# Kernel tuning notes

Hardware: AMD Instinct MI355X
Metric: run time of the kernel (lower is better)

The kernel has to match this reference:

```python
import jax, jax.numpy as jnp
import numpy as np

N, D, DEG, DEPTH, H = 50000, 300, 6, 3, 4
E = N * DEG
DK = D // H


def setup_inputs() -> dict:
    key = jax.random.key(0)
    ks = jax.random.split(key, 14)
    # circulant molecular-like graph: node i <-> i+k (k=1,2,3), edges emitted in
    # reverse pairs (2t, 2t+1) as required by reverse_edge()
    u = np.arange(N)
    src_l, dst_l = [], []
    for k in (1, 2, 3):
        v = (u + k) % N
        src_l.append(np.stack([u, v], 1).reshape(-1))
        dst_l.append(np.stack([v, u], 1).reshape(-1))
    src = np.concatenate(src_l).astype(np.int32)
    dst = np.concatenate(dst_l).astype(np.int32)
    # incoming-edge ids per node (every node has exactly DEG in-edges)
    order = np.argsort(dst, kind='stable')
    nbr_eids = order.reshape(N, DEG).astype(np.int32)
    nbr_mask = np.ones((N, DEG), dtype=bool)
    sd = 1.0 / np.sqrt(D)
    p = lambda i, shape: jax.random.normal(ks[i], shape, jnp.float32) * sd
    return {
        'f': jax.random.normal(ks[0], (N, D), jnp.float32),
        'x': jax.random.normal(ks[1], (E, D), jnp.float32),
        'Wq': p(2, (D, D)), 'bq': jnp.zeros((D,), jnp.float32),
        'Wk': p(3, (D, D)), 'bk': jnp.zeros((D,), jnp.float32),
        'Wv': p(4, (D, D)), 'bv': jnp.zeros((D,), jnp.float32),
        'Wo': p(5, (D, D)), 'bo': jnp.zeros((D,), jnp.float32),
        'W_mp': p(6, (DEPTH - 1, D, D)), 'b_mp': jnp.zeros((DEPTH - 1, D), jnp.float32),
        'W_last': p(7, (3 * D, D)), 'b_last': jnp.zeros((D,), jnp.float32),
        'src': jnp.asarray(src), 'dst': jnp.asarray(dst),
        'nbr_eids': jnp.asarray(nbr_eids), 'nbr_mask': jnp.asarray(nbr_mask),
    }


def reference(f, x, Wq, bq, Wk, bk, Wv, bv, Wo, bo, W_mp, b_mp, W_last, b_last,
              src, dst, nbr_eids, nbr_mask):
    n = f.shape[0]
    e = x.shape[0]
    rev = jnp.arange(e) ^ 1                     # reverse-pair permutation
    has_in = nbr_mask.any(axis=-1)              # [N]
    scale = 1.0 / jnp.sqrt(jnp.float32(DK))
    h = x                                       # edge state 'h' init from 'x'
    f_h = f                                     # node state 'f_h' init from 'f'
    for i in range(DEPTH - 1):
        # ragged mailbox of incoming edge states, padded to DEG
        m = jnp.where(nbr_mask[..., None], h[nbr_eids], 0.0)        # [N,DEG,D]
        q = (f_h @ Wq + bq).reshape(n, H, DK)                        # query = node feat
        k = (m @ Wk + bk).reshape(n, DEG, H, DK)                     # key   = mailbox
        v = ((m + f_h[:, None, :]) @ Wv + bv).reshape(n, DEG, H, DK) # value = mailbox + feat
        scores = jnp.einsum('nhk,ndhk->nhd', q, k) * scale          # [N,H,DEG]
        scores = jnp.where(nbr_mask[:, None, :], scores, -1e9)
        attn = jax.nn.softmax(scores, axis=-1)
        out = jnp.einsum('nhd,ndhk->nhk', attn, v).reshape(n, D) @ Wo + bo
        f_h = jnp.where(has_in[:, None], out, f_h)
        # edge update: m = f_h[src] - rev_h; h = relu(x + Linear_i(m))
        m_e = f_h[src] - h[rev]
        h = jax.nn.relu(x + m_e @ W_mp[i] + b_mp[i])
    # GEANet is undefined in the provided source -> identity pass-through
    mail = jax.ops.segment_sum(h, dst, num_segments=n)              # sum of in-edge states
    f_new = jnp.concatenate([mail, f_h, f], axis=-1) @ W_last + b_last
    f_final = jnp.where(has_in[:, None], f_new, f_h)
    return f_final, h
```

## Files before the change

kernel.cpp:

```cpp
#include <hip/hip_runtime.h>
#include <hip/hip_bf16.h>

typedef unsigned long long ull;
typedef unsigned int u32;
typedef unsigned short u16;
typedef __hip_bfloat16 bf16;
typedef __attribute__((ext_vector_type(8))) short v8s;
typedef __attribute__((ext_vector_type(4))) float v4f;
typedef __attribute__((ext_vector_type(2))) ull v2u;

#define NN 50000
#define DD 300
#define PD 320
#define EE (NN*6)

__device__ __forceinline__ u16 f2bf(float f) {
    u32 u = __float_as_uint(f);
    u32 r = u + 0x7FFFu + ((u >> 16) & 1u);
    return (u16)(r >> 16);
}
__device__ __forceinline__ u32 cvtpk(float lo, float hi) {
    u32 r;
    asm("v_cvt_pk_bf16_f32 %0, %1, %2" : "=v"(r) : "v"(lo), "v"(hi));
    return r;
}
__device__ __forceinline__ float lo16(u32 u) { return __uint_as_float(u << 16); }
__device__ __forceinline__ float hi16(u32 u) { return __uint_as_float(u & 0xffff0000u); }

__device__ __forceinline__ u32 sub2bf(u32 a, u32 b) {
    return cvtpk(lo16(a) - lo16(b), hi16(a) - hi16(b));
}
__device__ __forceinline__ ull sub4bf(ull a, ull b) {
    u32 l = sub2bf((u32)a, (u32)b);
    u32 h = sub2bf((u32)(a >> 32), (u32)(b >> 32));
    return (ull)l | ((ull)h << 32);
}

enum { A_DIR = 0, A_MPG = 1, A_CAT = 2 };
enum { E_BIAS = 0, E_RELUX = 1 };
enum { O_F32 = 1, O_BF16 = 2, O_BOTH = 3 };

template<int AMODE, int EPI, int OUTM, int NW, int NSEG>
__global__ __launch_bounds__(NW*64)
void gemm_mfma(const bf16* __restrict__ A0, const bf16* __restrict__ A1,
               const bf16* __restrict__ A2, const bf16* __restrict__ A3,
               const bf16* __restrict__ A4,
               const int* __restrict__ srcidx, const bf16* __restrict__ BT,
               const float* __restrict__ bias0, const float* __restrict__ bias1,
               const bf16* __restrict__ xepi,
               float* __restrict__ Cf, bf16* __restrict__ Cb0, bf16* __restrict__ Cb1,
               int M, int ybias, long ycb)
{
    __shared__ __align__(16) char Als[64 * 640];
    const int tid = threadIdx.x;
    const int wave = tid >> 6, lane = tid & 63;
    const int l15 = lane & 15, l4 = lane >> 4;
    const int wv = (NW == 8) ? (wave & 3) : wave;
    const int half = (NW == 8) ? (wave >> 2) : 0;
    const int rowBase = blockIdx.x * 64;
    const int T = NW * 64;
    const int gy = blockIdx.y;
    BT += (long)gy * 204800;
    if (bias0) bias0 += (long)gy * ybias;
    if (bias1) bias1 += (long)gy * ybias;
    if (Cb0) Cb0 += gy * ycb;
    if (Cb1) Cb1 += gy * ycb;

    v4f acc[4][5];
    const v4f vzero = {0.f, 0.f, 0.f, 0.f};
    #pragma unroll
    for (int mt = 0; mt < 4; ++mt)
        #pragma unroll
        for (int nt = 0; nt < 5; ++nt) acc[mt][nt] = vzero;

    for (int seg = 0; seg < NSEG; ++seg) {
        const bf16* As = (seg == 0) ? A0 : (seg == 1 ? A1 : (seg == 2 ? A2 :
                         (seg == 3 ? A3 : A4)));
        if (seg) __syncthreads();
        #pragma unroll
        for (int s = 0; s < 2560 / T; ++s) {
            int c = tid + T * s;
            int r = c / 40, ch = c - r * 40;
            int grow = rowBase + r;
            int gc = (grow < M) ? grow : 0;
            v2u v;
            if (AMODE == A_MPG) {
                int s0 = srcidx[gc];
                v2u a = *(const v2u*)(A0 + (long)s0 * PD + ch * 8);
                v2u b = *(const v2u*)(A1 + (long)(gc ^ 1) * PD + ch * 8);
                v[0] = sub4bf(a[0], b[0]);
                v[1] = sub4bf(a[1], b[1]);
            } else {
                v = *(const v2u*)(As + (long)gc * PD + ch * 8);
            }
            *(v2u*)(Als + ((c * 16) ^ ((r & 7) << 4))) = v;
        }
        __syncthreads();

        const bf16* BTs = BT + (long)seg * 320 * PD;
        #pragma unroll
        for (int ks = 0; ks < 10; ++ks) {
            v8s af[4];
            #pragma unroll
            for (int mt = 0; mt < 4; ++mt) {
                int rowL = mt * 16 + l15;
                af[mt] = *(const v8s*)(Als +
                    ((rowL * 640 + ks * 64 + l4 * 16) ^ ((rowL & 7) << 4)));
            }
            #pragma unroll
            for (int nt = 0; nt < 5; ++nt) {
                int col = wave * 80 + nt * 16 + l15;
                v8s bfr = *(const v8s*)(BTs + (long)col * PD + ks * 32 + l4 * 8);
                #pragma unroll
                for (int mt = 0; mt < 4; ++mt)
                    acc[mt][nt] = __builtin_amdgcn_mfma_f32_16x16x32_bf16(
                        af[mt], bfr, acc[mt][nt], 0, 0, 0);
            }
        }
        if (seg + 1 < NSEG) __syncthreads();
    }

    const int NOUT = (NW == 8) ? 2 : 1;
    #pragma unroll
    for (int oh = 0; oh < NOUT; ++oh) {
        __syncthreads();
        if (half == oh) {
            const float* bias = oh ? bias1 : bias0;
            #pragma unroll
            for (int nt = 0; nt < 5; ++nt) {
                int col = wv * 80 + nt * 16 + l15;
                float bvv = bias ? bias[col] : 0.f;
                #pragma unroll
                for (int mt = 0; mt < 4; ++mt) {
                    #pragma unroll
                    for (int r = 0; r < 4; ++r) {
                        int rowL = mt * 16 + l4 * 4 + r;
                        *(u16*)(Als + ((rowL * 640 + col * 2) ^ (((rowL >> 2) & 7) << 4)))
                            = f2bf(acc[mt][nt][r] + bvv);
                    }
                }
            }
        }
        __syncthreads();
        {
            bf16* Cb = oh ? Cb1 : Cb0;
            #pragma unroll
            for (int s = 0; s < 2560 / T; ++s) {
                int c = tid + T * s;
                int r = c / 40, ch = c - r * 40;
                int grow = rowBase + r;
                if (grow >= M) continue;
                v2u val = *(const v2u*)(Als + ((c * 16) ^ (((r >> 2) & 7) << 4)));
                if (EPI == E_RELUX) {
                    v2u xv = *(const v2u*)(xepi + (long)grow * PD + ch * 8);
                    #pragma unroll
                    for (int w = 0; w < 2; ++w) {
                        u32 a0 = (u32)val[w], a1 = (u32)(val[w] >> 32);
                        u32 x0 = (u32)xv[w],  x1 = (u32)(xv[w] >> 32);
                        u32 r0 = cvtpk(fmaxf(lo16(a0) + lo16(x0), 0.f),
                                       fmaxf(hi16(a0) + hi16(x0), 0.f));
                        u32 r1 = cvtpk(fmaxf(lo16(a1) + lo16(x1), 0.f),
                                       fmaxf(hi16(a1) + hi16(x1), 0.f));
                        val[w] = (ull)r0 | ((ull)r1 << 32);
                    }
                }
                if (OUTM & O_BF16)
                    *(v2u*)(Cb + (long)grow * PD + ch * 8) = val;
                if (OUTM & O_F32) {
                    int col0 = ch * 8;
                    if (col0 < DD) {
                        u32 a0 = (u32)val[0], a1 = (u32)(val[0] >> 32);
                        float4 lo = {lo16(a0), hi16(a0), lo16(a1), hi16(a1)};
                        *(float4*)(Cf + (long)grow * DD + col0) = lo;
                        if (col0 + 4 < DD) {
                            u32 b0 = (u32)val[1], b1 = (u32)(val[1] >> 32);
                            float4 hi = {lo16(b0), hi16(b0), lo16(b1), hi16(b1)};
                            *(float4*)(Cf + (long)grow * DD + col0 + 4) = hi;
                        }
                    }
                }
            }
        }
    }
}

__global__ __launch_bounds__(256)
void scoreU_k(const bf16* __restrict__ G0, const bf16* __restrict__ G1,
              const bf16* __restrict__ G2, const bf16* __restrict__ G3,
              const bf16* __restrict__ h, const int* __restrict__ nbr,
              bf16* __restrict__ U0, bf16* __restrict__ U1,
              bf16* __restrict__ U2, bf16* __restrict__ U3)
{
    int wave = threadIdx.x >> 6, lane = threadIdx.x & 63;
    int n = blockIdx.x * 4 + wave;
    if (n >= NN) return;
    int eid[6];
    #pragma unroll
    for (int d = 0; d < 6; ++d) eid[d] = nbr[n * 6 + d];

    bool act = lane < 40;
    int cl = act ? lane : 0;
    long go = (long)n * PD + cl * 8;

    float g[4][8];
    #pragma unroll
    for (int hh = 0; hh < 4; ++hh) {
        const bf16* Gp = (hh == 0) ? G0 : (hh == 1) ? G1 : (hh == 2) ? G2 : G3;
        v2u gv = *(const v2u*)(Gp + go);
        u32 w0 = (u32)gv[0], w1 = (u32)(gv[0] >> 32);
        u32 w2 = (u32)gv[1], w3 = (u32)(gv[1] >> 32);
        g[hh][0] = lo16(w0); g[hh][1] = hi16(w0);
        g[hh][2] = lo16(w1); g[hh][3] = hi16(w1);
        g[hh][4] = lo16(w2); g[hh][5] = hi16(w2);
        g[hh][6] = lo16(w3); g[hh][7] = hi16(w3);
        if (!act)
            #pragma unroll
            for (int i = 0; i < 8; ++i) g[hh][i] = 0.f;
    }
    v2u hp[6];
    #pragma unroll
    for (int d = 0; d < 6; ++d)
        hp[d] = *(const v2u*)(h + (long)eid[d] * PD + cl * 8);

    float s0[6], s1[6], s2[6], s3[6];
    #pragma unroll
    for (int d = 0; d < 6; ++d) {
        u32 w0 = (u32)hp[d][0], w1 = (u32)(hp[d][0] >> 32);
        u32 w2 = (u32)hp[d][1], w3 = (u32)(hp[d][1] >> 32);
        float hf[8] = {lo16(w0), hi16(w0), lo16(w1), hi16(w1),
                       lo16(w2), hi16(w2), lo16(w3), hi16(w3)};
        float p0 = 0, p1 = 0, p2 = 0, p3 = 0;
        #pragma unroll
        for (int i = 0; i < 8; ++i) {
            p0 += g[0][i] * hf[i];
            p1 += g[1][i] * hf[i];
            p2 += g[2][i] * hf[i];
            p3 += g[3][i] * hf[i];
        }
        #pragma unroll
        for (int off = 32; off; off >>= 1) {
            p0 += __shfl_xor(p0, off);
            p1 += __shfl_xor(p1, off);
            p2 += __shfl_xor(p2, off);
            p3 += __shfl_xor(p3, off);
        }
        s0[d] = p0; s1[d] = p1; s2[d] = p2; s3[d] = p3;
    }

    const float scale = 0.1154700538379252f;
    float at[4][6];
    {
        float m0 = -1e30f, m1 = -1e30f, m2 = -1e30f, m3 = -1e30f;
        #pragma unroll
        for (int d = 0; d < 6; ++d) {
            s0[d] *= scale; s1[d] *= scale; s2[d] *= scale; s3[d] *= scale;
            m0 = fmaxf(m0, s0[d]); m1 = fmaxf(m1, s1[d]);
            m2 = fmaxf(m2, s2[d]); m3 = fmaxf(m3, s3[d]);
        }
        float t0 = 0, t1 = 0, t2 = 0, t3 = 0;
        #pragma unroll
        for (int d = 0; d < 6; ++d) {
            at[0][d] = expf(s0[d] - m0); t0 += at[0][d];
            at[1][d] = expf(s1[d] - m1); t1 += at[1][d];
            at[2][d] = expf(s2[d] - m2); t2 += at[2][d];
            at[3][d] = expf(s3[d] - m3); t3 += at[3][d];
        }
        t0 = 1.f / t0; t1 = 1.f / t1; t2 = 1.f / t2; t3 = 1.f / t3;
        #pragma unroll
        for (int d = 0; d < 6; ++d) {
            at[0][d] *= t0; at[1][d] *= t1; at[2][d] *= t2; at[3][d] *= t3;
        }
    }

    float u[4][8];
    #pragma unroll
    for (int hh = 0; hh < 4; ++hh)
        #pragma unroll
        for (int i = 0; i < 8; ++i) u[hh][i] = 0.f;
    #pragma unroll
    for (int d = 0; d < 6; ++d) {
        u32 w0 = (u32)hp[d][0], w1 = (u32)(hp[d][0] >> 32);
        u32 w2 = (u32)hp[d][1], w3 = (u32)(hp[d][1] >> 32);
        float hf[8] = {lo16(w0), hi16(w0), lo16(w1), hi16(w1),
                       lo16(w2), hi16(w2), lo16(w3), hi16(w3)};
        #pragma unroll
        for (int i = 0; i < 8; ++i) {
            u[0][i] += at[0][d] * hf[i];
            u[1][i] += at[1][d] * hf[i];
            u[2][i] += at[2][d] * hf[i];
            u[3][i] += at[3][d] * hf[i];
        }
    }
    if (act) {
        #pragma unroll
        for (int hh = 0; hh < 4; ++hh) {
            bf16* Up = (hh == 0) ? U0 : (hh == 1) ? U1 : (hh == 2) ? U2 : U3;
            v2u r;
            r[0] = (ull)cvtpk(u[hh][0], u[hh][1]) |
                   ((ull)cvtpk(u[hh][2], u[hh][3]) << 32);
            r[1] = (ull)cvtpk(u[hh][4], u[hh][5]) |
                   ((ull)cvtpk(u[hh][6], u[hh][7]) << 32);
            *(v2u*)(Up + go) = r;
        }
    }
}

__global__ __launch_bounds__(256)
void mailf_k(const float* __restrict__ h, const int* __restrict__ nbr,
             bf16* __restrict__ mail)
{
    int idx = blockIdx.x * 256 + threadIdx.x;
    if (idx >= NN * 80) return;
    int n = idx / 80, c4 = idx - n * 80;
    float4 s = {0.f, 0.f, 0.f, 0.f};
    if (c4 < 75) {
        const int* e = nbr + n * 6;
        #pragma unroll
        for (int d = 0; d < 6; ++d) {
            float4 v = *(const float4*)(h + (long)e[d] * DD + c4 * 4);
            s.x += v.x; s.y += v.y; s.z += v.z; s.w += v.w;
        }
    }
    ull r = (ull)cvtpk(s.x, s.y) | ((ull)cvtpk(s.z, s.w) << 32);
    *(ull*)(mail + (long)n * PD + c4 * 4) = r;
}

__global__ __launch_bounds__(256)
void conv_k(const float* __restrict__ in, bf16* __restrict__ out, int rows)
{
    long idx = (long)blockIdx.x * 256 + threadIdx.x;
    if (idx >= (long)rows * 40) return;
    int r = (int)(idx / 40), ch = (int)(idx - (long)r * 40);
    int c4 = ch * 2;
    float4 a = {0, 0, 0, 0}, b = {0, 0, 0, 0};
    if (c4 < 75)     a = *(const float4*)(in + (long)r * DD + c4 * 4);
    if (c4 + 1 < 75) b = *(const float4*)(in + (long)r * DD + c4 * 4 + 4);
    v2u v;
    v[0] = (ull)cvtpk(a.x, a.y) | ((ull)cvtpk(a.z, a.w) << 32);
    v[1] = (ull)cvtpk(b.x, b.y) | ((ull)cvtpk(b.z, b.w) << 32);
    *(v2u*)(out + (long)r * PD + ch * 8) = v;
}

__global__ __launch_bounds__(256)
void tw_k(const float* __restrict__ W, bf16* __restrict__ BT)
{
    int idx = blockIdx.x * 256 + threadIdx.x;
    if (idx >= 320 * 320) return;
    int nn = idx / 320, kk = idx - nn * 320;
    u16 v = 0;
    if (nn < DD && kk < DD) v = f2bf(W[kk * DD + nn]);
    ((u16*)BT)[idx] = v;
}

__global__ __launch_bounds__(256)
void twf_k(const float* __restrict__ W, float* __restrict__ WT)
{
    __shared__ float t[32][33];
    int bx = blockIdx.x % 10, by = blockIdx.x / 10;
    int r0 = by * 32, c0 = bx * 32;
    int tx = threadIdx.x & 31, ty = threadIdx.x >> 5;
    #pragma unroll
    for (int i = 0; i < 4; ++i) {
        int r = r0 + ty + i * 8, c = c0 + tx;
        t[ty + i * 8][tx] = (r < DD && c < DD) ? W[r * DD + c] : 0.f;
    }
    __syncthreads();
    #pragma unroll
    for (int i = 0; i < 4; ++i)
        WT[(c0 + ty + i * 8) * 320 + r0 + tx] = t[tx][ty + i * 8];
}

__global__ __launch_bounds__(256)
void wqk_k(const float* __restrict__ WqT, const float* __restrict__ Wk,
           bf16* __restrict__ slab)
{
    int idx = blockIdx.x * 256 + threadIdx.x;
    if (idx >= 1280 * 320) return;
    int c = idx / 320, k = idx - c * 320;
    int hh = c / 320;
    int ci = c - hh * 320;
    float v = 0.f;
    if (ci < DD && k < DD) {
        int jb = hh * 75;
        for (int j = 0; j < 75; ++j)
            v += WqT[(jb + j) * 320 + k] * Wk[ci * DD + jb + j];
    }
    ((u16*)slab)[idx] = f2bf(v);
}

__global__ __launch_bounds__(256)
void wcomp_k(const float* __restrict__ WvT, const float* __restrict__ Wo,
             bf16* __restrict__ slab)
{
    int idx = blockIdx.x * 256 + threadIdx.x;
    if (idx >= 5 * 320 * 320) return;
    int s = idx / 102400, rem = idx - s * 102400;
    int c = rem / 320, k = rem - c * 320;
    float v = 0.f;
    if (c < DD && k < DD) {
        int jb = (s < 4) ? s * 75 : 0;
        int jn = (s < 4) ? 75 : 300;
        for (int j = 0; j < jn; ++j)
            v += WvT[(jb + j) * 320 + k] * Wo[(jb + j) * DD + c];
    }
    ((u16*)slab)[idx] = f2bf(v);
}

__global__ void bias_k(const float* __restrict__ WkT, const float* __restrict__ Wo,
                       const float* __restrict__ bq, const float* __restrict__ bv,
                       const float* __restrict__ bo, const float* __restrict__ bmp,
                       const float* __restrict__ blast, float* __restrict__ outb)
{
    int a = blockIdx.x, i = threadIdx.x;
    float v = 0.f;
    if (i < DD) {
        if (a < 4) {
            for (int j = 0; j < 75; ++j)
                v += bq[a * 75 + j] * WkT[(a * 75 + j) * 320 + i];
        } else if (a == 4) {
            for (int j = 0; j < DD; ++j) v += bv[j] * Wo[j * DD + i];
            v += bo[i];
        } else if (a == 5) v = bmp[i];
        else if (a == 6) v = bmp[DD + i];
        else v = blast[i];
    }
    outb[a * 320 + i] = v;
}

extern "C" void kernel_launch(void* const* d_in, const int* in_sizes, int n_in,
                              void* d_out, int out_size, void* d_ws, size_t ws_size,
                              hipStream_t stream)
{
    const float* f     = (const float*)d_in[0];
    const float* x     = (const float*)d_in[1];
    const float* Wq    = (const float*)d_in[2];
    const float* bq    = (const float*)d_in[3];
    const float* Wk    = (const float*)d_in[4];
    const float* bv    = (const float*)d_in[7];
    const float* Wv    = (const float*)d_in[6];
    const float* Wo    = (const float*)d_in[8];
    const float* bo    = (const float*)d_in[9];
    const float* Wmp   = (const float*)d_in[10];
    const float* bmp   = (const float*)d_in[11];
    const float* Wlast = (const float*)d_in[12];
    const float* blast = (const float*)d_in[13];
    const int*   src   = (const int*)d_in[14];
    const int*   nbr   = (const int*)d_in[16];

    float* out     = (float*)d_out;
    float* f_final = out;
    float* h_final = out + (long)NN * DD;

    char* ws = (char*)d_ws;
    bf16* xb  = (bf16*)(ws);
    bf16* h1b = (bf16*)(ws + 192000000LL);
    bf16* fb  = (bf16*)(ws + 576000000LL);
    bf16* G0  = (bf16*)(ws + 608000000LL);
    bf16* G1  = (bf16*)(ws + 640000000LL);
    bf16* G2  = (bf16*)(ws + 672000000LL);
    bf16* G3  = (bf16*)(ws + 704000000LL);
    bf16* FHb = (bf16*)(ws + 736000000LL);
    bf16* WT  = (bf16*)(ws + 768000000LL);
    float* BIAS = (float*)(ws + 772000000LL);
    float* WqT  = (float*)(ws + 772100000LL);
    float* WkT  = (float*)(ws + 772600000LL);
    float* WvT  = (float*)(ws + 773100000LL);
    auto slot = [&](int i) { return WT + (long)i * 320 * 320; };
    bf16* qk   = slot(0);
    bf16* fh5  = slot(4);
    bf16* mp0  = slot(9);
    bf16* mp1  = slot(10);
    bf16* lst  = slot(11);
    float* g0p = BIAS;          float* g1p = BIAS + 320;
    float* b2p = BIAS + 1280;
    float* bm0p = BIAS + 1600;  float* bm1p = BIAS + 1920;
    float* blp = BIAS + 2240;
    bf16* MLb = G0;

    dim3 blk(256), blk8(512);
    const int gN = (NN + 63) / 64;
    const int gE = (EE + 63) / 64;

    conv_k<<<(int)(((long)EE * 40 + 255) / 256), blk, 0, stream>>>(x, xb, EE);
    conv_k<<<(int)(((long)NN * 40 + 255) / 256), blk, 0, stream>>>(f, fb, NN);
    twf_k<<<100, blk, 0, stream>>>(Wq, WqT);
    twf_k<<<100, blk, 0, stream>>>(Wk, WkT);
    twf_k<<<100, blk, 0, stream>>>(Wv, WvT);
    wqk_k<<<1600, blk, 0, stream>>>(WqT, Wk, qk);
    wcomp_k<<<2000, blk, 0, stream>>>(WvT, Wo, fh5);
    tw_k<<<400, blk, 0, stream>>>(Wmp, mp0);
    tw_k<<<400, blk, 0, stream>>>(Wmp + 90000, mp1);
    tw_k<<<400, blk, 0, stream>>>(Wlast, lst);
    tw_k<<<400, blk, 0, stream>>>(Wlast + 90000, slot(12));
    tw_k<<<400, blk, 0, stream>>>(Wlast + 180000, slot(13));
    bias_k<<<8, 320, 0, stream>>>(WkT, Wo, bq, bv, bo, bmp, blast, BIAS);

    for (int it = 0; it < 2; ++it) {
        const bf16* hb  = it ? h1b : xb;
        const bf16* fhb = it ? FHb : fb;
        gemm_mfma<A_DIR, E_BIAS, O_BF16, 8, 1><<<dim3(gN, 2), blk8, 0, stream>>>(
            fhb, nullptr, nullptr, nullptr, nullptr, nullptr, qk,
            g0p, g1p, nullptr, nullptr, G0, G1, NN, 640, 32000000);
        scoreU_k<<<(NN + 3) / 4, blk, 0, stream>>>(G0, G1, G2, G3, hb, nbr,
                                                   G0, G1, G2, G3);
        gemm_mfma<A_CAT, E_BIAS, O_BF16, 4, 5><<<gN, blk, 0, stream>>>(
            G0, G1, G2, G3, fhb, nullptr, fh5, b2p, nullptr, nullptr,
            nullptr, FHb, nullptr, NN, 0, 0);
        if (it == 0) {
            gemm_mfma<A_MPG, E_RELUX, O_BF16, 4, 1><<<gE, blk, 0, stream>>>(
                FHb, hb, nullptr, nullptr, nullptr, src, mp0, bm0p, nullptr,
                xb, nullptr, h1b, nullptr, EE, 0, 0);
        } else {
            gemm_mfma<A_MPG, E_RELUX, O_F32, 4, 1><<<gE, blk, 0, stream>>>(
                FHb, hb, nullptr, nullptr, nullptr, src, mp1, bm1p, nullptr,
                xb, h_final, nullptr, nullptr, EE, 0, 0);
        }
    }

    mailf_k<<<(NN * 80 + 255) / 256, blk, 0, stream>>>(h_final, nbr, MLb);
    gemm_mfma<A_CAT, E_BIAS, O_F32, 4, 3><<<gN, blk, 0, stream>>>(
        MLb, FHb, fb, nullptr, nullptr, nullptr, lst, blp, nullptr, nullptr,
        f_final, nullptr, nullptr, NN, 0, 0);
}
```

Measured before the change: 2.151 ms.

## Load GEMM A-tiles via global_load_lds and split edge subtraction into two K segments

The A-operand staging in the GEMM kernel now uses direct global-to-LDS loads (global_load_lds, 16 bytes per lane) with the XOR swizzle applied on the global address side, instead of loading into registers and then storing to LDS. The edge update's f_h[src] - h[rev] subtraction is no longer computed during staging. It becomes a two-segment GEMM against W and a sign-flipped copy of W, with gather modes selecting src-indexed or reverse-paired rows. This removes VGPR round trips and the bf16 subtract/convert work, but doubles the K dimension and the MFMA work of the edge GEMMs. It also drops the trailing barrier between segments and rearranges the workspace offsets.

Measured after the change: 2.606 ms. +21.2%, slower.

```diff
diff --git a/kernel.cpp b/kernel.cpp
--- a/kernel.cpp
+++ b/kernel.cpp
@@ -27,25 +27,23 @@
 __device__ __forceinline__ float lo16(u32 u) { return __uint_as_float(u << 16); }
 __device__ __forceinline__ float hi16(u32 u) { return __uint_as_float(u & 0xffff0000u); }
 
-__device__ __forceinline__ u32 sub2bf(u32 a, u32 b) {
-    return cvtpk(lo16(a) - lo16(b), hi16(a) - hi16(b));
-}
-__device__ __forceinline__ ull sub4bf(ull a, ull b) {
-    u32 l = sub2bf((u32)a, (u32)b);
-    u32 h = sub2bf((u32)(a >> 32), (u32)(b >> 32));
-    return (ull)l | ((ull)h << 32);
-}
-
-enum { A_DIR = 0, A_MPG = 1, A_CAT = 2 };
+__device__ __forceinline__ void gl16(const void* g, void* l) {
+    __builtin_amdgcn_global_load_lds(
+        (const __attribute__((address_space(1))) u32*)g,
+        (__attribute__((address_space(3))) u32*)l, 16, 0, 0);
+}
+
 enum { E_BIAS = 0, E_RELUX = 1 };
-enum { O_F32 = 1, O_BF16 = 2, O_BOTH = 3 };
-
-template<int AMODE, int EPI, int OUTM, int NW, int NSEG>
+enum { O_F32 = 1, O_BF16 = 2 };
+enum { GM_LIN = 0, GM_SRC = 1, GM_REV = 2 };
+
+template<int EPI, int OUTM, int NW, int NSEG>
 __global__ __launch_bounds__(NW*64)
 void gemm_mfma(const bf16* __restrict__ A0, const bf16* __restrict__ A1,
                const bf16* __restrict__ A2, const bf16* __restrict__ A3,
                const bf16* __restrict__ A4,
-               const int* __restrict__ srcidx, const bf16* __restrict__ BT,
+               const int* __restrict__ srcidx, int gmodes,
+               const bf16* __restrict__ BT,
                const float* __restrict__ bias0, const float* __restrict__ bias1,
                const bf16* __restrict__ xepi,
                float* __restrict__ Cf, bf16* __restrict__ Cb0, bf16* __restrict__ Cb1,
@@ -76,24 +74,19 @@
     for (int seg = 0; seg < NSEG; ++seg) {
         const bf16* As = (seg == 0) ? A0 : (seg == 1 ? A1 : (seg == 2 ? A2 :
                          (seg == 3 ? A3 : A4)));
+        const int gm = (gmodes >> (seg * 3)) & 7;
         if (seg) __syncthreads();
         #pragma unroll
         for (int s = 0; s < 2560 / T; ++s) {
             int c = tid + T * s;
             int r = c / 40, ch = c - r * 40;
-            int grow = rowBase + r;
-            int gc = (grow < M) ? grow : 0;
-            v2u v;
-            if (AMODE == A_MPG) {
-                int s0 = srcidx[gc];
-                v2u a = *(const v2u*)(A0 + (long)s0 * PD + ch * 8);
-                v2u b = *(const v2u*)(A1 + (long)(gc ^ 1) * PD + ch * 8);
-                v[0] = sub4bf(a[0], b[0]);
-                v[1] = sub4bf(a[1], b[1]);
-            } else {
-                v = *(const v2u*)(As + (long)gc * PD + ch * 8);
-            }
-            *(v2u*)(Als + ((c * 16) ^ ((r & 7) << 4))) = v;
+            int gc = rowBase + r;
+            gc = (gc < M) ? gc : (M - 1);
+            int row = (gm == GM_SRC) ? srcidx[gc] :
+                      ((gm == GM_REV) ? (gc ^ 1) : gc);
+            int chs = ((ch * 16) ^ ((r & 7) << 4)) >> 4;
+            int lbase = (c - lane) * 16;
+            gl16(As + (long)row * PD + chs * 8, Als + lbase);
         }
         __syncthreads();
 
@@ -117,7 +110,6 @@
                         af[mt], bfr, acc[mt][nt], 0, 0, 0);
             }
         }
-        if (seg + 1 < NSEG) __syncthreads();
     }
 
     const int NOUT = (NW == 8) ? 2 : 1;
@@ -342,13 +334,13 @@
 }
 
 __global__ __launch_bounds__(256)
-void tw_k(const float* __restrict__ W, bf16* __restrict__ BT)
+void tw_k(const float* __restrict__ W, bf16* __restrict__ BT, float sgn)
 {
     int idx = blockIdx.x * 256 + threadIdx.x;
     if (idx >= 320 * 320) return;
     int nn = idx / 320, kk = idx - nn * 320;
     u16 v = 0;
-    if (nn < DD && kk < DD) v = f2bf(W[kk * DD + nn]);
+    if (nn < DD && kk < DD) v = f2bf(sgn * W[kk * DD + nn]);
     ((u16*)BT)[idx] = v;
 }
 
@@ -461,16 +453,13 @@
     bf16* G3  = (bf16*)(ws + 704000000LL);
     bf16* FHb = (bf16*)(ws + 736000000LL);
     bf16* WT  = (bf16*)(ws + 768000000LL);
-    float* BIAS = (float*)(ws + 772000000LL);
-    float* WqT  = (float*)(ws + 772100000LL);
-    float* WkT  = (float*)(ws + 772600000LL);
-    float* WvT  = (float*)(ws + 773100000LL);
+    float* BIAS = (float*)(ws + 771300000LL);
+    float* WqT  = (float*)(ws + 771400000LL);
+    float* WkT  = (float*)(ws + 771850000LL);
+    float* WvT  = (float*)(ws + 772300000LL);
     auto slot = [&](int i) { return WT + (long)i * 320 * 320; };
     bf16* qk   = slot(0);
     bf16* fh5  = slot(4);
-    bf16* mp0  = slot(9);
-    bf16* mp1  = slot(10);
-    bf16* lst  = slot(11);
     float* g0p = BIAS;          float* g1p = BIAS + 320;
     float* b2p = BIAS + 1280;
     float* bm0p = BIAS + 1600;  float* bm1p = BIAS + 1920;
@@ -488,37 +477,41 @@
     twf_k<<<100, blk, 0, stream>>>(Wv, WvT);
     wqk_k<<<1600, blk, 0, stream>>>(WqT, Wk, qk);
     wcomp_k<<<2000, blk, 0, stream>>>(WvT, Wo, fh5);
-    tw_k<<<400, blk, 0, stream>>>(Wmp, mp0);
-    tw_k<<<400, blk, 0, stream>>>(Wmp + 90000, mp1);
-    tw_k<<<400, blk, 0, stream>>>(Wlast, lst);
-    tw_k<<<400, blk, 0, stream>>>(Wlast + 90000, slot(12));
-    tw_k<<<400, blk, 0, stream>>>(Wlast + 180000, slot(13));
+    tw_k<<<400, blk, 0, stream>>>(Wmp, slot(9), 1.f);
+    tw_k<<<400, blk, 0, stream>>>(Wmp, slot(10), -1.f);
+    tw_k<<<400, blk, 0, stream>>>(Wmp + 90000, slot(11), 1.f);
+    tw_k<<<400, blk, 0, stream>>>(Wmp + 90000, slot(12), -1.f);
+    tw_k<<<400, blk, 0, stream>>>(Wlast, slot(13), 1.f);
+    tw_k<<<400, blk, 0, stream>>>(Wlast + 90000, slot(14), 1.f);
+    tw_k<<<400, blk, 0, stream>>>(Wlast + 180000, slot(15), 1.f);
     bias_k<<<8, 320, 0, stream>>>(WkT, Wo, bq, bv, bo, bmp, blast, BIAS);
+
+    const int GM_MP = GM_SRC | (GM_REV << 3);
 
     for (int it = 0; it < 2; ++it) {
         const bf16* hb  = it ? h1b : xb;
         const bf16* fhb = it ? FHb : fb;
-        gemm_mfma<A_DIR, E_BIAS, O_BF16, 8, 1><<<dim3(gN, 2), blk8, 0, stream>>>(
-            fhb, nullptr, nullptr, nullptr, nullptr, nullptr, qk,
+        gemm_mfma<E_BIAS, O_BF16, 8, 1><<<dim3(gN, 2), blk8, 0, stream>>>(
+            fhb, nullptr, nullptr, nullptr, nullptr, nullptr, 0, qk,
             g0p, g1p, nullptr, nullptr, G0, G1, NN, 640, 32000000);
         scoreU_k<<<(NN + 3) / 4, blk, 0, stream>>>(G0, G1, G2, G3, hb, nbr,
                                                    G0, G1, G2, G3);
-        gemm_mfma<A_CAT, E_BIAS, O_BF16, 4, 5><<<gN, blk, 0, stream>>>(
-            G0, G1, G2, G3, fhb, nullptr, fh5, b2p, nullptr, nullptr,
+        gemm_mfma<E_BIAS, O_BF16, 4, 5><<<gN, blk, 0, stream>>>(
+            G0, G1, G2, G3, fhb, nullptr, 0, fh5, b2p, nullptr, nullptr,
             nullptr, FHb, nullptr, NN, 0, 0);
         if (it == 0) {
-            gemm_mfma<A_MPG, E_RELUX, O_BF16, 4, 1><<<gE, blk, 0, stream>>>(
-                FHb, hb, nullptr, nullptr, nullptr, src, mp0, bm0p, nullptr,
-                xb, nullptr, h1b, nullptr, EE, 0, 0);
+            gemm_mfma<E_RELUX, O_BF16, 4, 2><<<gE, blk, 0, stream>>>(
+                FHb, hb, nullptr, nullptr, nullptr, src, GM_MP, slot(9),
+                bm0p, nullptr, xb, nullptr, h1b, nullptr, EE, 0, 0);
         } else {
-            gemm_mfma<A_MPG, E_RELUX, O_F32, 4, 1><<<gE, blk, 0, stream>>>(
-                FHb, hb, nullptr, nullptr, nullptr, src, mp1, bm1p, nullptr,
-                xb, h_final, nullptr, nullptr, EE, 0, 0);
+            gemm_mfma<E_RELUX, O_F32, 4, 2><<<gE, blk, 0, stream>>>(
+                FHb, hb, nullptr, nullptr, nullptr, src, GM_MP, slot(11),
+                bm1p, nullptr, xb, h_final, nullptr, nullptr, EE, 0, 0);
         }
     }
 
     mailf_k<<<(NN * 80 + 255) / 256, blk, 0, stream>>>(h_final, nbr, MLb);
-    gemm_mfma<A_CAT, E_BIAS, O_F32, 4, 3><<<gN, blk, 0, stream>>>(
-        MLb, FHb, fb, nullptr, nullptr, nullptr, lst, blp, nullptr, nullptr,
-        f_final, nullptr, nullptr, NN, 0, 0);
-}
+    gemm_mfma<E_BIAS, O_F32, 4, 3><<<gN, blk, 0, stream>>>(
+        MLb, FHb, fb, nullptr, nullptr, nullptr, 0, slot(13), blp, nullptr,
+        nullptr, f_final, nullptr, nullptr, NN, 0, 0);
+}
```
